# Kernel tuning notes

Measured on AMD Instinct MI355X. Metric: run time of the kernel, lower is better.

The kernel has to match this reference:

```python
import jax, jax.numpy as jnp
import numpy as np
from jax import lax

# pywt Wavelet('db4') decomposition filters
DEC_LO = jnp.array([-0.010597401784997278, 0.032883011666982945, 0.030841381835986965,
                    -0.18703481171888114, -0.02798376941698385, 0.6308807679295904,
                    0.7148465705525415, 0.23037781330885523], dtype=jnp.float32)
DEC_HI = jnp.array([-0.23037781330885523, 0.7148465705525415, -0.6308807679295904,
                    -0.02798376941698385, 0.18703481171888114, 0.030841381835986965,
                    -0.032883011666982945, -0.010597401784997278], dtype=jnp.float32)


def dwt_level(x, lo, hi):
    # single-level pywt dwt, mode='symmetric', along last axis
    f = lo.shape[0]
    p = f - 1
    pad = [(0, 0)] * (x.ndim - 1) + [(p, p)]
    xe = jnp.pad(x, pad, mode='symmetric')[..., 1:]  # offset 1 matches pywt phase
    lead = x.shape[:-1]
    xin = xe.reshape(-1, 1, xe.shape[-1])            # [N,1,L]
    filt = jnp.stack([lo[::-1], hi[::-1]])[:, None, :]  # flip: true convolution, [2,1,f]
    out = lax.conv_general_dilated(xin, filt, (2,), 'VALID')  # [N,2,floor((n+f-1)/2)]
    cA = out[:, 0].reshape(lead + (-1,))
    cD = out[:, 1].reshape(lead + (-1,))
    return cA, cD


def wavedec4(x):
    # pywt.wavedec(x,'db4',level=4) concatenated: [cA4,cD4,cD3,cD2,cD1]
    details = []
    a = x
    for _ in range(4):
        a, d = dwt_level(a, DEC_LO, DEC_HI)
        details.append(d)
    return jnp.concatenate([a] + details[::-1], axis=-1)


def lstm_last(xs, w_ih, w_hh, b_ih, b_hh):
    # torch LSTM (gate order i,f,g,o); returns last timestep hidden state
    B, T, _ = xs.shape
    H = w_hh.shape[1]
    h0 = jnp.zeros((B, H), xs.dtype)
    c0 = jnp.zeros((B, H), xs.dtype)
    b = b_ih + b_hh

    def step(carry, x_t):
        h, c = carry
        gates = x_t @ w_ih.T + h @ w_hh.T + b
        i, f, g, o = jnp.split(gates, 4, axis=-1)
        c = jax.nn.sigmoid(f) * c + jax.nn.sigmoid(i) * jnp.tanh(g)
        h = jax.nn.sigmoid(o) * jnp.tanh(c)
        return (h, c), None

    (h, _), _ = lax.scan(step, (h0, c0), jnp.swapaxes(xs, 0, 1))
    return h


def setup_inputs() -> dict:
    key = jax.random.key(0)
    ks = jax.random.split(key, 9)
    B, S, T = 256, 1024, 21
    return {
        'x': jax.random.normal(ks[0], (B, S, T), jnp.float32),
        'conv_w': jax.random.normal(ks[1], (64, 78, 3), jnp.float32) * 0.06,
        'conv_b': jax.random.normal(ks[2], (64,), jnp.float32) * 0.06,
        'w_ih': jax.random.normal(ks[3], (128, 64), jnp.float32) * 0.12,
        'w_hh': jax.random.normal(ks[4], (128, 32), jnp.float32) * 0.17,
        'b_ih': jax.random.normal(ks[5], (128,), jnp.float32) * 0.17,
        'b_hh': jax.random.normal(ks[6], (128,), jnp.float32) * 0.17,
        'fc_w': jax.random.normal(ks[7], (1, 32), jnp.float32) * 0.17,
        'fc_b': jax.random.normal(ks[8], (1,), jnp.float32) * 0.17,
    }


def reference(x, conv_w, conv_b, w_ih, w_hh, b_ih, b_hh, fc_w, fc_b):
    freq = jnp.abs(jnp.fft.rfft(x, axis=2))          # [B,S,11]
    tf = wavedec4(x)                                 # [B,S,46]
    combined = jnp.concatenate([x, freq, tf], axis=2)  # [B,S,78]
    combined = jnp.swapaxes(combined, 1, 2)          # [B,78,S]
    y = lax.conv_general_dilated(combined, conv_w, (1,), [(1, 1)]) + conv_b[None, :, None]
    y = jax.nn.relu(y)
    B, C, S = y.shape
    y = y.reshape(B, C, S // 2, 2).max(axis=-1)      # max_pool1d(k=2,s=2)
    y = jnp.transpose(y, (0, 2, 1))                  # [B,S//2,64]
    h = lstm_last(y, w_ih, w_hh, b_ih, b_hh)         # [B,32]
    return h @ fc_w.T + fc_b                         # [B,1]
```

## Files before the change

kernel.cpp:

```cpp
#include <hip/hip_runtime.h>
#include <math.h>

typedef _Float16 half8 __attribute__((ext_vector_type(8)));
typedef float floatx16 __attribute__((ext_vector_type(16)));
typedef float float2v __attribute__((ext_vector_type(2)));

constexpr float L2E = 1.4426950408889634f;

constexpr float DLO[8] = {-0.010597401784997278f, 0.032883011666982945f, 0.030841381835986965f,
                          -0.18703481171888114f, -0.02798376941698385f, 0.6308807679295904f,
                          0.7148465705525415f, 0.23037781330885523f};
constexpr float DHI[8] = {-0.23037781330885523f, 0.7148465705525415f, -0.6308807679295904f,
                          -0.02798376941698385f, 0.18703481171888114f, 0.030841381835986965f,
                          -0.032883011666982945f, -0.010597401784997278f};

constexpr float CT21[21] = {
  1.0f,          0.95557281f,  0.82623877f,  0.62348980f,  0.36534102f,  0.07473009f,
  -0.22252093f, -0.5f,        -0.73305187f, -0.90096887f, -0.98883083f,
  -0.98883083f, -0.90096887f, -0.73305187f, -0.5f,        -0.22252093f,
  0.07473009f,   0.36534102f,  0.62348980f,  0.82623877f,  0.95557281f};
constexpr float ST21[21] = {
  0.0f,          0.29475517f,  0.56332006f,  0.78183148f,  0.93087375f,  0.99720380f,
  0.97492791f,   0.86602540f,  0.68017274f,  0.43388374f,  0.14904227f,
  -0.14904227f, -0.43388374f, -0.68017274f, -0.86602540f, -0.97492791f,
  -0.99720380f, -0.93087375f, -0.78183148f, -0.56332006f, -0.29475517f};

template<int N>
__device__ __forceinline__ void dwt_step(const float* in, float* a, float* d) {
  constexpr int NO = (N + 7) / 2;
#pragma unroll
  for (int i = 0; i < NO; i++) {
    float sa = 0.f, sd = 0.f;
#pragma unroll
    for (int j = 0; j < 8; j++) {
      int rel = 2 * i + j - 6;
      int idx = (rel < 0) ? (-rel - 1) : ((rel >= N) ? (2 * N - rel - 1) : rel);
      float v = in[idx];
      sa = fmaf(v, DLO[7 - j], sa);
      sd = fmaf(v, DHI[7 - j], sd);
    }
    a[i] = sa;
    d[i] = sd;
  }
}

__device__ __forceinline__ void gload_lds16(const void* g, void* l) {
  __builtin_amdgcn_global_load_lds(
      (const __attribute__((address_space(1))) unsigned int*)g,
      (__attribute__((address_space(3))) unsigned int*)l, 16, 0, 0);
}

__device__ __forceinline__ void feature_row(const float* __restrict__ xr,
                                            _Float16* hrow) {
  float xx[21];
#pragma unroll
  for (int t = 0; t < 21; t++) xx[t] = xr[t];

#pragma unroll
  for (int i = 78; i < 88; i++) hrow[i] = (_Float16)0.f;

#pragma unroll
  for (int t = 0; t < 21; t++) hrow[t] = (_Float16)xx[t];

#pragma unroll
  for (int k = 0; k < 11; k++) {
    float re = 0.f, im = 0.f;
#pragma unroll
    for (int t = 0; t < 21; t++) {
      const int m = (k * t) % 21;
      re = fmaf(xx[t], CT21[m], re);
      im = fmaf(xx[t], ST21[m], im);
    }
    hrow[21 + k] = (_Float16)sqrtf(re * re + im * im);
  }

  float a1[14], d1[14];
  dwt_step<21>(xx, a1, d1);
#pragma unroll
  for (int i = 0; i < 14; i++) hrow[64 + i] = (_Float16)d1[i];
  float a2[10], d2[10];
  dwt_step<14>(a1, a2, d2);
#pragma unroll
  for (int i = 0; i < 10; i++) hrow[54 + i] = (_Float16)d2[i];
  float a3[8], d3[8];
  dwt_step<10>(a2, a3, d3);
#pragma unroll
  for (int i = 0; i < 8; i++) hrow[46 + i] = (_Float16)d3[i];
  float a4[7], d4[7];
  dwt_step<8>(a3, a4, d4);
#pragma unroll
  for (int i = 0; i < 7; i++) {
    hrow[32 + i] = (_Float16)a4[i];
    hrow[39 + i] = (_Float16)d4[i];
  }
}

__global__ __launch_bounds__(256) void wprep_kernel(const float* __restrict__ cw,
                                                    const float* __restrict__ w_ih,
                                                    const float* __restrict__ b_ih,
                                                    const float* __restrict__ b_hh,
                                                    _Float16* __restrict__ WbT,
                                                    _Float16* __restrict__ wih16,
                                                    float* __restrict__ biasI) {
  int idx = blockIdx.x * 256 + threadIdx.x;
  if (idx < 64 * 264) {
    int o = idx / 264, k = idx - o * 264;
    float v = 0.f;
    if (k < 240) {
      int dk = k / 80, c = k - dk * 80;
      if (c < 78) v = cw[o * 234 + c * 3 + dk];
    }
    WbT[idx] = (_Float16)v;
  } else if (idx < 16896 + 8192) {
    int j = idx - 16896;
    wih16[j] = (_Float16)(L2E * w_ih[j]);
  } else if (idx < 16896 + 8192 + 128) {
    int g = idx - 16896 - 8192;
    int p = ((g & 63) << 1) | (g >> 6);
    biasI[p] = L2E * (b_ih[g] + b_hh[g]);
  }
}

__global__ __launch_bounds__(256, 2) void conv_proj_kernel(const float* __restrict__ x,
                                                           const _Float16* __restrict__ WbT,
                                                           const float* __restrict__ cbias,
                                                           const _Float16* __restrict__ wih16,
                                                           const float* __restrict__ biasI,
                                                           float* __restrict__ Xp) {
  __shared__ __align__(16) char smem[61184];
  _Float16* At = (_Float16*)smem;
  _Float16* Bt = (_Float16*)(smem + 24576);
  _Float16* yt = (_Float16*)smem;
  _Float16* wl = (_Float16*)(smem + 9216);
  float* biasl = (float*)(smem + 27648);
  float* Xpt   = (float*)(smem + 28160);
  float* bl    = (float*)(smem + 60928);

  const int tid = threadIdx.x;
  const int b = blockIdx.y;
  const int s0 = blockIdx.x * 128;
  const int T0 = blockIdx.x * 64;

  {
    const char* srcB = (const char*)WbT;
#pragma unroll
    for (int i = 0; i < 8; i++) {
      const int idx = i * 256 + tid;
      gload_lds16(srcB + (size_t)idx * 16, (char*)Bt + (size_t)idx * 16);
    }
    if (tid < 64)
      gload_lds16(srcB + (size_t)(2048 + tid) * 16, (char*)Bt + (size_t)(2048 + tid) * 16);
  }
  if (tid < 64) bl[tid] = cbias[tid];

  if (tid < 130) {
    const int s = s0 - 1 + tid;
    __align__(16) _Float16 hrow[88];
    if (s < 0 || s > 1023) {
#pragma unroll
      for (int i = 0; i < 88; i++) hrow[i] = (_Float16)0.f;
    } else {
      feature_row(x + ((size_t)(b << 10) + s) * 21, hrow);
    }
    uint4* dst = (uint4*)&At[tid * 88];
    const uint4* src = (const uint4*)hrow;
#pragma unroll
    for (int i = 0; i < 11; i++) dst[i] = src[i];
  }
  __syncthreads();

  const int wave = tid >> 6, lane = tid & 63;
  const int ml = lane & 31;
  const int kg = lane >> 5;
  const int am = wave * 32 + ml;

  floatx16 acc0 = {};
  floatx16 acc1 = {};
#pragma unroll
  for (int ks = 0; ks < 15; ks++) {
    const int kb = ks * 16 + kg * 8;
    const int dk = (kb >= 160) ? 2 : ((kb >= 80) ? 1 : 0);
    const int c = kb - dk * 80;
    half8 av = *(const half8*)&At[(am + dk) * 88 + c];
    half8 bv0 = *(const half8*)&Bt[ml * 264 + kb];
    half8 bv1 = *(const half8*)&Bt[(32 + ml) * 264 + kb];
    acc0 = __builtin_amdgcn_mfma_f32_32x32x16_f16(av, bv0, acc0, 0, 0, 0);
    acc1 = __builtin_amdgcn_mfma_f32_32x32x16_f16(av, bv1, acc1, 0, 0, 0);
  }

  const float b0 = bl[ml], b1 = bl[32 + ml];
  float v0s[8], v1s[8];
#pragma unroll
  for (int p = 0; p < 8; p++) {
    v0s[p] = fmaxf(fmaxf(acc0[2 * p], acc0[2 * p + 1]) + b0, 0.f);
    v1s[p] = fmaxf(fmaxf(acc1[2 * p], acc1[2 * p + 1]) + b1, 0.f);
  }

  __syncthreads();

#pragma unroll
  for (int p = 0; p < 8; p++) {
    const int toff = (p & 1) + ((p >> 1) << 2);
    const int t = wave * 16 + (kg << 1) + toff;
    yt[t * 72 + ml] = (_Float16)v0s[p];
    yt[t * 72 + 32 + ml] = (_Float16)v1s[p];
  }
  for (int i = tid; i < 2048; i += 256) {
    int g = i >> 4, c4 = i & 15;
    *(uint2*)(wl + g * 72 + c4 * 4) = *(const uint2*)(wih16 + g * 64 + c4 * 4);
  }
  if (tid < 128) biasl[tid] = biasI[tid];
  __syncthreads();

  const int tm = wave & 1, tn0 = (wave >> 1) * 2;
  floatx16 pa0 = {};
  floatx16 pa1 = {};
#pragma unroll
  for (int kq = 0; kq < 4; kq++) {
    const int k0 = kq * 16 + kg * 8;
    half8 av = *(const half8*)&yt[(tm * 32 + ml) * 72 + k0];
    half8 bv0 = *(const half8*)&wl[(tn0 * 32 + ml) * 72 + k0];
    half8 bv1 = *(const half8*)&wl[((tn0 + 1) * 32 + ml) * 72 + k0];
    pa0 = __builtin_amdgcn_mfma_f32_32x32x16_f16(av, bv0, pa0, 0, 0, 0);
    pa1 = __builtin_amdgcn_mfma_f32_32x32x16_f16(av, bv1, pa1, 0, 0, 0);
  }

  {
    const int g0i = tn0 * 32 + ml;
    const int p0 = ((g0i & 63) << 1) | (g0i >> 6);
    const int g1i = (tn0 + 1) * 32 + ml;
    const int p1 = ((g1i & 63) << 1) | (g1i >> 6);
#pragma unroll
    for (int reg = 0; reg < 16; reg++) {
      const int row = (reg & 3) + 8 * (reg >> 2) + 4 * kg;
      const int m = tm * 32 + row;
      Xpt[m * 128 + p0] = pa0[reg];
      Xpt[m * 128 + p1] = pa1[reg];
    }
  }
  __syncthreads();

  float* xpg = Xp + ((size_t)b * 512 + T0) * 128;
  for (int i = tid; i < 2048; i += 256) {
    const int r = i >> 5, c4 = (i & 31) << 2;
    float4 v = *(float4*)&Xpt[r * 128 + c4];
    float4 bb = *(float4*)&biasl[c4];
    v.x += bb.x; v.y += bb.y; v.z += bb.z; v.w += bb.w;
    *(float4*)&xpg[r * 128 + c4] = v;
  }
}

__device__ __forceinline__ float bcast_lane(float v, int k) {
  return __uint_as_float(__builtin_amdgcn_readlane(__float_as_uint(v), k));
}

#if __has_builtin(__builtin_amdgcn_exp2f)
#define EXP2F __builtin_amdgcn_exp2f
#else
#define EXP2F exp2f
#endif

#if __has_builtin(__builtin_amdgcn_permlane32_swap)
__device__ __forceinline__ float swap_half(float x) {
  auto r = __builtin_amdgcn_permlane32_swap(__float_as_uint(x), __float_as_uint(x),
                                            false, false);
  return __uint_as_float(r[1]);
}
#else
__device__ __forceinline__ float swap_half(float x) { return __shfl_down(x, 32); }
#endif

__device__ __forceinline__ void lstm_step(float& h, float& c, float2v xg,
                                          const float* __restrict__ wA,
                                          const float* __restrict__ wB, bool lo) {
  float hs[32];
#pragma unroll
  for (int k = 0; k < 32; k++) hs[k] = bcast_lane(h, k);

  float aA0 = xg.x, aA1 = 0.f, aB0 = xg.y, aB1 = 0.f;
#pragma unroll
  for (int k = 0; k < 32; k += 2) {
    aA0 = fmaf(hs[k], wA[k], aA0);
    aB0 = fmaf(hs[k], wB[k], aB0);
    aA1 = fmaf(hs[k + 1], wA[k + 1], aA1);
    aB1 = fmaf(hs[k + 1], wB[k + 1], aB1);
  }
  const float gA = aA0 + aA1;
  const float gB = aB0 + aB1;

  float sA = __builtin_amdgcn_rcpf(1.0f + EXP2F(-gA));

  float argB = lo ? (gB + gB) : (-gB);
  float rB = __builtin_amdgcn_rcpf(EXP2F(argB) + 1.0f);
  float sB = lo ? fmaf(-2.f, rB, 1.f) : rB;

  float fv = swap_half(sA);
  float ov = swap_half(sB);
  c = fmaf(fv, c, sA * sB);
  float rc = __builtin_amdgcn_rcpf(EXP2F(c * (2.f * L2E)) + 1.0f);
  float ov2 = ov + ov;
  h = fmaf(-ov2, rc, ov);
}

__global__ __launch_bounds__(64, 1)
__attribute__((amdgpu_waves_per_eu(1, 1)))
void lstm_fc_kernel(const float* __restrict__ Xp,
                    const float* __restrict__ w_hh,
                    const float* __restrict__ fc_w,
                    const float* __restrict__ fc_b,
                    float* __restrict__ out) {
  const int b = blockIdx.x;
  const int L = threadIdx.x;
  const bool lo = (L < 32);

  float wA[32], wB[32];
  {
    const float4* rA = (const float4*)(w_hh + L * 32);
    const float4* rB = (const float4*)(w_hh + (L + 64) * 32);
#pragma unroll
    for (int q = 0; q < 8; q++) {
      float4 a4 = rA[q], b4 = rB[q];
      wA[4 * q + 0] = L2E * a4.x; wA[4 * q + 1] = L2E * a4.y;
      wA[4 * q + 2] = L2E * a4.z; wA[4 * q + 3] = L2E * a4.w;
      wB[4 * q + 0] = L2E * b4.x; wB[4 * q + 1] = L2E * b4.y;
      wB[4 * q + 2] = L2E * b4.z; wB[4 * q + 3] = L2E * b4.w;
    }
  }

  const float* xp = Xp + (size_t)b * 512 * 128;
  float h = 0.f, c = 0.f;

  float2v p2[4];
#pragma unroll
  for (int u = 0; u < 4; u++) p2[u] = *(const float2v*)&xp[u * 128 + 2 * L];

  for (int t0 = 0; t0 < 512; t0 += 4) {
    float2v c2[4];
#pragma unroll
    for (int u = 0; u < 4; u++) c2[u] = p2[u];
    if (t0 + 4 < 512) {
#pragma unroll
      for (int u = 0; u < 4; u++)
        p2[u] = *(const float2v*)&xp[(t0 + 4 + u) * 128 + 2 * L];
    }
#pragma unroll
    for (int u = 0; u < 4; u++) lstm_step(h, c, c2[u], wA, wB, lo);
  }

  float v = lo ? h * fc_w[L & 31] : 0.f;
#pragma unroll
  for (int off = 32; off > 0; off >>= 1) v += __shfl_down(v, off);
  if (L == 0) out[b] = v + fc_b[0];
}

extern "C" void kernel_launch(void* const* d_in, const int* in_sizes, int n_in,
                              void* d_out, int out_size, void* d_ws, size_t ws_size,
                              hipStream_t stream) {
  const float* x      = (const float*)d_in[0];
  const float* conv_w = (const float*)d_in[1];
  const float* conv_b = (const float*)d_in[2];
  const float* w_ih   = (const float*)d_in[3];
  const float* w_hh   = (const float*)d_in[4];
  const float* b_ih   = (const float*)d_in[5];
  const float* b_hh   = (const float*)d_in[6];
  const float* fc_w   = (const float*)d_in[7];
  const float* fc_b   = (const float*)d_in[8];
  float* out = (float*)d_out;

  char* wsb = (char*)d_ws;
  float*    Xp    = (float*)wsb;
  _Float16* WbT   = (_Float16*)(wsb + 67108864);
  _Float16* wih16 = (_Float16*)(wsb + 67108864 + 33792);
  float*    biasI = (float*)(wsb + 67108864 + 33792 + 16384);

  wprep_kernel<<<dim3(99), dim3(256), 0, stream>>>(conv_w, w_ih, b_ih, b_hh,
                                                   WbT, wih16, biasI);
  conv_proj_kernel<<<dim3(8, 256), dim3(256), 0, stream>>>(x, WbT, conv_b,
                                                           wih16, biasI, Xp);
  lstm_fc_kernel<<<dim3(256), dim3(64), 0, stream>>>(Xp, w_hh, fc_w, fc_b, out);
}
```

Baseline: 224.8 us.

## Fuse conv/projection and LSTM into one producer-consumer kernel per batch

Merges the conv+pool+input-projection kernel and the LSTM kernel into a single per-batch workgroup. Three producer waves compute 64-timestep chunks of projected gates while one consumer wave runs the LSTM recurrence on completed chunks, signalled through LDS atomic counters. The aim is to hide the conv/projection work behind the serial LSTM and drop a kernel launch. In exchange, the producer work for each batch now runs on three waves instead of eight blocks, and the sync relies on spin-waits and global-memory visibility within the workgroup.

Measured after the change: 199.4 us. -11.3%, faster.

```diff
diff --git a/kernel.cpp b/kernel.cpp
--- a/kernel.cpp
+++ b/kernel.cpp
@@ -121,13 +121,82 @@
   }
 }
 
-__global__ __launch_bounds__(256, 2) void conv_proj_kernel(const float* __restrict__ x,
-                                                           const _Float16* __restrict__ WbT,
-                                                           const float* __restrict__ cbias,
-                                                           const _Float16* __restrict__ wih16,
-                                                           const float* __restrict__ biasI,
-                                                           float* __restrict__ Xp) {
+__device__ __forceinline__ float bcast_lane(float v, int k) {
+  return __uint_as_float(__builtin_amdgcn_readlane(__float_as_uint(v), k));
+}
+
+#if __has_builtin(__builtin_amdgcn_exp2f)
+#define EXP2F __builtin_amdgcn_exp2f
+#else
+#define EXP2F exp2f
+#endif
+
+#if __has_builtin(__builtin_amdgcn_permlane32_swap)
+__device__ __forceinline__ float swap_half(float x) {
+  auto r = __builtin_amdgcn_permlane32_swap(__float_as_uint(x), __float_as_uint(x),
+                                            false, false);
+  return __uint_as_float(r[1]);
+}
+#else
+__device__ __forceinline__ float swap_half(float x) { return __shfl_down(x, 32); }
+#endif
+
+__device__ __forceinline__ void lstm_step(float& h, float& c, float2v xg,
+                                          const float* __restrict__ wA,
+                                          const float* __restrict__ wB, bool lo) {
+  float hs[32];
+#pragma unroll
+  for (int k = 0; k < 32; k++) hs[k] = bcast_lane(h, k);
+
+  float aA0 = xg.x, aA1 = 0.f, aB0 = xg.y, aB1 = 0.f;
+#pragma unroll
+  for (int k = 0; k < 32; k += 2) {
+    aA0 = fmaf(hs[k], wA[k], aA0);
+    aB0 = fmaf(hs[k], wB[k], aB0);
+    aA1 = fmaf(hs[k + 1], wA[k + 1], aA1);
+    aB1 = fmaf(hs[k + 1], wB[k + 1], aB1);
+  }
+  const float gA = aA0 + aA1;
+  const float gB = aB0 + aB1;
+
+  float sA = __builtin_amdgcn_rcpf(1.0f + EXP2F(-gA));
+
+  float argB = lo ? (gB + gB) : (-gB);
+  float rB = __builtin_amdgcn_rcpf(EXP2F(argB) + 1.0f);
+  float sB = lo ? fmaf(-2.f, rB, 1.f) : rB;
+
+  float fv = swap_half(sA);
+  float ov = swap_half(sB);
+  c = fmaf(fv, c, sA * sB);
+  float rc = __builtin_amdgcn_rcpf(EXP2F(c * (2.f * L2E)) + 1.0f);
+  float ov2 = ov + ov;
+  h = fmaf(-ov2, rc, ov);
+}
+
+__device__ __forceinline__ void prod_barrier(int* pb, int& target) {
+  target += 3;
+  __builtin_amdgcn_s_waitcnt(0);
+  if ((threadIdx.x & 63) == 0)
+    __hip_atomic_fetch_add(pb, 1, __ATOMIC_RELEASE, __HIP_MEMORY_SCOPE_WORKGROUP);
+  while (__hip_atomic_load(pb, __ATOMIC_ACQUIRE, __HIP_MEMORY_SCOPE_WORKGROUP) < target) {
+  }
+}
+
+__global__ __launch_bounds__(256, 1)
+__attribute__((amdgpu_waves_per_eu(1, 1)))
+void fused_kernel(const float* __restrict__ x,
+                  const _Float16* __restrict__ WbT,
+                  const float* __restrict__ cbias,
+                  const _Float16* __restrict__ wih16,
+                  const float* __restrict__ biasI,
+                  const float* __restrict__ w_hh,
+                  const float* __restrict__ fc_w,
+                  const float* __restrict__ fc_b,
+                  float* __restrict__ Xp,
+                  float* __restrict__ out) {
   __shared__ __align__(16) char smem[61184];
+  __shared__ int ready;
+  __shared__ int pbar;
   _Float16* At = (_Float16*)smem;
   _Float16* Bt = (_Float16*)(smem + 24576);
   _Float16* yt = (_Float16*)smem;
@@ -137,220 +206,166 @@
   float* bl    = (float*)(smem + 60928);
 
   const int tid = threadIdx.x;
-  const int b = blockIdx.y;
-  const int s0 = blockIdx.x * 128;
-  const int T0 = blockIdx.x * 64;
-
-  {
-    const char* srcB = (const char*)WbT;
-#pragma unroll
-    for (int i = 0; i < 8; i++) {
-      const int idx = i * 256 + tid;
-      gload_lds16(srcB + (size_t)idx * 16, (char*)Bt + (size_t)idx * 16);
-    }
-    if (tid < 64)
-      gload_lds16(srcB + (size_t)(2048 + tid) * 16, (char*)Bt + (size_t)(2048 + tid) * 16);
-  }
+  const int b = blockIdx.x;
+
+  if (tid == 0) { ready = 0; pbar = 0; }
   if (tid < 64) bl[tid] = cbias[tid];
-
-  if (tid < 130) {
-    const int s = s0 - 1 + tid;
-    __align__(16) _Float16 hrow[88];
-    if (s < 0 || s > 1023) {
-#pragma unroll
-      for (int i = 0; i < 88; i++) hrow[i] = (_Float16)0.f;
-    } else {
-      feature_row(x + ((size_t)(b << 10) + s) * 21, hrow);
-    }
-    uint4* dst = (uint4*)&At[tid * 88];
-    const uint4* src = (const uint4*)hrow;
-#pragma unroll
-    for (int i = 0; i < 11; i++) dst[i] = src[i];
-  }
   __syncthreads();
 
-  const int wave = tid >> 6, lane = tid & 63;
-  const int ml = lane & 31;
-  const int kg = lane >> 5;
-  const int am = wave * 32 + ml;
-
-  floatx16 acc0 = {};
-  floatx16 acc1 = {};
-#pragma unroll
-  for (int ks = 0; ks < 15; ks++) {
-    const int kb = ks * 16 + kg * 8;
-    const int dk = (kb >= 160) ? 2 : ((kb >= 80) ? 1 : 0);
-    const int c = kb - dk * 80;
-    half8 av = *(const half8*)&At[(am + dk) * 88 + c];
-    half8 bv0 = *(const half8*)&Bt[ml * 264 + kb];
-    half8 bv1 = *(const half8*)&Bt[(32 + ml) * 264 + kb];
-    acc0 = __builtin_amdgcn_mfma_f32_32x32x16_f16(av, bv0, acc0, 0, 0, 0);
-    acc1 = __builtin_amdgcn_mfma_f32_32x32x16_f16(av, bv1, acc1, 0, 0, 0);
-  }
-
-  const float b0 = bl[ml], b1 = bl[32 + ml];
-  float v0s[8], v1s[8];
-#pragma unroll
-  for (int p = 0; p < 8; p++) {
-    v0s[p] = fmaxf(fmaxf(acc0[2 * p], acc0[2 * p + 1]) + b0, 0.f);
-    v1s[p] = fmaxf(fmaxf(acc1[2 * p], acc1[2 * p + 1]) + b1, 0.f);
-  }
-
-  __syncthreads();
-
-#pragma unroll
-  for (int p = 0; p < 8; p++) {
-    const int toff = (p & 1) + ((p >> 1) << 2);
-    const int t = wave * 16 + (kg << 1) + toff;
-    yt[t * 72 + ml] = (_Float16)v0s[p];
-    yt[t * 72 + 32 + ml] = (_Float16)v1s[p];
-  }
-  for (int i = tid; i < 2048; i += 256) {
-    int g = i >> 4, c4 = i & 15;
-    *(uint2*)(wl + g * 72 + c4 * 4) = *(const uint2*)(wih16 + g * 64 + c4 * 4);
-  }
-  if (tid < 128) biasl[tid] = biasI[tid];
-  __syncthreads();
-
-  const int tm = wave & 1, tn0 = (wave >> 1) * 2;
-  floatx16 pa0 = {};
-  floatx16 pa1 = {};
-#pragma unroll
-  for (int kq = 0; kq < 4; kq++) {
-    const int k0 = kq * 16 + kg * 8;
-    half8 av = *(const half8*)&yt[(tm * 32 + ml) * 72 + k0];
-    half8 bv0 = *(const half8*)&wl[(tn0 * 32 + ml) * 72 + k0];
-    half8 bv1 = *(const half8*)&wl[((tn0 + 1) * 32 + ml) * 72 + k0];
-    pa0 = __builtin_amdgcn_mfma_f32_32x32x16_f16(av, bv0, pa0, 0, 0, 0);
-    pa1 = __builtin_amdgcn_mfma_f32_32x32x16_f16(av, bv1, pa1, 0, 0, 0);
-  }
-
-  {
-    const int g0i = tn0 * 32 + ml;
-    const int p0 = ((g0i & 63) << 1) | (g0i >> 6);
-    const int g1i = (tn0 + 1) * 32 + ml;
-    const int p1 = ((g1i & 63) << 1) | (g1i >> 6);
-#pragma unroll
-    for (int reg = 0; reg < 16; reg++) {
-      const int row = (reg & 3) + 8 * (reg >> 2) + 4 * kg;
-      const int m = tm * 32 + row;
-      Xpt[m * 128 + p0] = pa0[reg];
-      Xpt[m * 128 + p1] = pa1[reg];
-    }
-  }
-  __syncthreads();
-
-  float* xpg = Xp + ((size_t)b * 512 + T0) * 128;
-  for (int i = tid; i < 2048; i += 256) {
-    const int r = i >> 5, c4 = (i & 31) << 2;
-    float4 v = *(float4*)&Xpt[r * 128 + c4];
-    float4 bb = *(float4*)&biasl[c4];
-    v.x += bb.x; v.y += bb.y; v.z += bb.z; v.w += bb.w;
-    *(float4*)&xpg[r * 128 + c4] = v;
-  }
-}
-
-__device__ __forceinline__ float bcast_lane(float v, int k) {
-  return __uint_as_float(__builtin_amdgcn_readlane(__float_as_uint(v), k));
-}
-
-#if __has_builtin(__builtin_amdgcn_exp2f)
-#define EXP2F __builtin_amdgcn_exp2f
-#else
-#define EXP2F exp2f
-#endif
-
-#if __has_builtin(__builtin_amdgcn_permlane32_swap)
-__device__ __forceinline__ float swap_half(float x) {
-  auto r = __builtin_amdgcn_permlane32_swap(__float_as_uint(x), __float_as_uint(x),
-                                            false, false);
-  return __uint_as_float(r[1]);
-}
-#else
-__device__ __forceinline__ float swap_half(float x) { return __shfl_down(x, 32); }
-#endif
-
-__device__ __forceinline__ void lstm_step(float& h, float& c, float2v xg,
-                                          const float* __restrict__ wA,
-                                          const float* __restrict__ wB, bool lo) {
-  float hs[32];
-#pragma unroll
-  for (int k = 0; k < 32; k++) hs[k] = bcast_lane(h, k);
-
-  float aA0 = xg.x, aA1 = 0.f, aB0 = xg.y, aB1 = 0.f;
-#pragma unroll
-  for (int k = 0; k < 32; k += 2) {
-    aA0 = fmaf(hs[k], wA[k], aA0);
-    aB0 = fmaf(hs[k], wB[k], aB0);
-    aA1 = fmaf(hs[k + 1], wA[k + 1], aA1);
-    aB1 = fmaf(hs[k + 1], wB[k + 1], aB1);
-  }
-  const float gA = aA0 + aA1;
-  const float gB = aB0 + aB1;
-
-  float sA = __builtin_amdgcn_rcpf(1.0f + EXP2F(-gA));
-
-  float argB = lo ? (gB + gB) : (-gB);
-  float rB = __builtin_amdgcn_rcpf(EXP2F(argB) + 1.0f);
-  float sB = lo ? fmaf(-2.f, rB, 1.f) : rB;
-
-  float fv = swap_half(sA);
-  float ov = swap_half(sB);
-  c = fmaf(fv, c, sA * sB);
-  float rc = __builtin_amdgcn_rcpf(EXP2F(c * (2.f * L2E)) + 1.0f);
-  float ov2 = ov + ov;
-  h = fmaf(-ov2, rc, ov);
-}
-
-__global__ __launch_bounds__(64, 1)
-__attribute__((amdgpu_waves_per_eu(1, 1)))
-void lstm_fc_kernel(const float* __restrict__ Xp,
-                    const float* __restrict__ w_hh,
-                    const float* __restrict__ fc_w,
-                    const float* __restrict__ fc_b,
-                    float* __restrict__ out) {
-  const int b = blockIdx.x;
-  const int L = threadIdx.x;
-  const bool lo = (L < 32);
-
-  float wA[32], wB[32];
-  {
-    const float4* rA = (const float4*)(w_hh + L * 32);
-    const float4* rB = (const float4*)(w_hh + (L + 64) * 32);
-#pragma unroll
-    for (int q = 0; q < 8; q++) {
-      float4 a4 = rA[q], b4 = rB[q];
-      wA[4 * q + 0] = L2E * a4.x; wA[4 * q + 1] = L2E * a4.y;
-      wA[4 * q + 2] = L2E * a4.z; wA[4 * q + 3] = L2E * a4.w;
-      wB[4 * q + 0] = L2E * b4.x; wB[4 * q + 1] = L2E * b4.y;
-      wB[4 * q + 2] = L2E * b4.z; wB[4 * q + 3] = L2E * b4.w;
-    }
-  }
-
-  const float* xp = Xp + (size_t)b * 512 * 128;
-  float h = 0.f, c = 0.f;
-
-  float2v p2[4];
-#pragma unroll
-  for (int u = 0; u < 4; u++) p2[u] = *(const float2v*)&xp[u * 128 + 2 * L];
-
-  for (int t0 = 0; t0 < 512; t0 += 4) {
-    float2v c2[4];
-#pragma unroll
-    for (int u = 0; u < 4; u++) c2[u] = p2[u];
-    if (t0 + 4 < 512) {
-#pragma unroll
-      for (int u = 0; u < 4; u++)
-        p2[u] = *(const float2v*)&xp[(t0 + 4 + u) * 128 + 2 * L];
-    }
-#pragma unroll
-    for (int u = 0; u < 4; u++) lstm_step(h, c, c2[u], wA, wB, lo);
-  }
-
-  float v = lo ? h * fc_w[L & 31] : 0.f;
-#pragma unroll
-  for (int off = 32; off > 0; off >>= 1) v += __shfl_down(v, off);
-  if (L == 0) out[b] = v + fc_b[0];
+  if (tid < 64) {
+    const int L = tid;
+    const bool lo = (L < 32);
+    float wA[32], wB[32];
+    {
+      const float4* rA = (const float4*)(w_hh + L * 32);
+      const float4* rB = (const float4*)(w_hh + (L + 64) * 32);
+#pragma unroll
+      for (int q = 0; q < 8; q++) {
+        float4 a4 = rA[q], b4 = rB[q];
+        wA[4 * q + 0] = L2E * a4.x; wA[4 * q + 1] = L2E * a4.y;
+        wA[4 * q + 2] = L2E * a4.z; wA[4 * q + 3] = L2E * a4.w;
+        wB[4 * q + 0] = L2E * b4.x; wB[4 * q + 1] = L2E * b4.y;
+        wB[4 * q + 2] = L2E * b4.z; wB[4 * q + 3] = L2E * b4.w;
+      }
+    }
+
+    float h = 0.f, c = 0.f;
+    for (int k = 0; k < 8; k++) {
+      while (__hip_atomic_load(&ready, __ATOMIC_ACQUIRE, __HIP_MEMORY_SCOPE_WORKGROUP) < k + 1)
+        __builtin_amdgcn_s_sleep(2);
+      const float* xp = Xp + ((size_t)b * 512 + (size_t)k * 64) * 128;
+      float2v p2[4];
+#pragma unroll
+      for (int u = 0; u < 4; u++) p2[u] = *(const float2v*)&xp[u * 128 + 2 * L];
+      for (int t0 = 0; t0 < 64; t0 += 4) {
+        float2v c2[4];
+#pragma unroll
+        for (int u = 0; u < 4; u++) c2[u] = p2[u];
+        if (t0 + 4 < 64) {
+#pragma unroll
+          for (int u = 0; u < 4; u++)
+            p2[u] = *(const float2v*)&xp[(t0 + 4 + u) * 128 + 2 * L];
+        }
+#pragma unroll
+        for (int u = 0; u < 4; u++) lstm_step(h, c, c2[u], wA, wB, lo);
+      }
+    }
+
+    float v = lo ? h * fc_w[L & 31] : 0.f;
+#pragma unroll
+    for (int off = 32; off > 0; off >>= 1) v += __shfl_down(v, off);
+    if (L == 0) out[b] = v + fc_b[0];
+  } else {
+    const int ptid = tid - 64;
+    const int pw = (tid >> 6) - 1;
+    const int lane = tid & 63, ml = lane & 31, kg = lane >> 5;
+    int bt = 0;
+
+    for (int k = 0; k < 8; k++) {
+      const int s0 = k * 128;
+
+      {
+        const char* srcB = (const char*)WbT;
+#pragma unroll
+        for (int j = 0; j < 11; j++) {
+          const int idx = j * 192 + ptid;
+          gload_lds16(srcB + (size_t)idx * 16, (char*)Bt + (size_t)idx * 16);
+        }
+      }
+      if (ptid < 130) {
+        const int s = s0 - 1 + ptid;
+        __align__(16) _Float16 hrow[88];
+        if (s < 0 || s > 1023) {
+#pragma unroll
+          for (int i = 0; i < 88; i++) hrow[i] = (_Float16)0.f;
+        } else {
+          feature_row(x + ((size_t)(b << 10) + s) * 21, hrow);
+        }
+        uint4* dst = (uint4*)&At[ptid * 88];
+        const uint4* src = (const uint4*)hrow;
+#pragma unroll
+        for (int i = 0; i < 11; i++) dst[i] = src[i];
+      }
+      prod_barrier(&pbar, bt);
+
+      float pooled[3][8];
+      {
+        int cc = 0;
+        for (int wt = pw; wt < 8; wt += 3, cc++) {
+          const int mt = wt & 3, nt = wt >> 2;
+          floatx16 acc = {};
+#pragma unroll
+          for (int ks = 0; ks < 15; ks++) {
+            const int kb = ks * 16 + kg * 8;
+            const int dk = (kb >= 160) ? 2 : ((kb >= 80) ? 1 : 0);
+            const int cofs = kb - dk * 80;
+            half8 av = *(const half8*)&At[(mt * 32 + ml + dk) * 88 + cofs];
+            half8 bv = *(const half8*)&Bt[(nt * 32 + ml) * 264 + kb];
+            acc = __builtin_amdgcn_mfma_f32_32x32x16_f16(av, bv, acc, 0, 0, 0);
+          }
+          const float bo = bl[nt * 32 + ml];
+#pragma unroll
+          for (int p = 0; p < 8; p++)
+            pooled[cc][p] = fmaxf(fmaxf(acc[2 * p], acc[2 * p + 1]) + bo, 0.f);
+        }
+      }
+      prod_barrier(&pbar, bt);
+
+      {
+        int cc = 0;
+        for (int wt = pw; wt < 8; wt += 3, cc++) {
+          const int mt = wt & 3, nt = wt >> 2;
+#pragma unroll
+          for (int p = 0; p < 8; p++) {
+            const int toff = (p & 1) + ((p >> 1) << 2);
+            const int t = mt * 16 + (kg << 1) + toff;
+            yt[t * 72 + nt * 32 + ml] = (_Float16)pooled[cc][p];
+          }
+        }
+        for (int i = ptid; i < 2048; i += 192) {
+          int g = i >> 4, c4 = i & 15;
+          *(uint2*)(wl + g * 72 + c4 * 4) = *(const uint2*)(wih16 + g * 64 + c4 * 4);
+        }
+        if (ptid < 128) biasl[ptid] = biasI[ptid];
+      }
+      prod_barrier(&pbar, bt);
+
+      for (int wt = pw; wt < 8; wt += 3) {
+        const int pm = wt & 1, pn = wt >> 1;
+        floatx16 pa = {};
+#pragma unroll
+        for (int kq = 0; kq < 4; kq++) {
+          const int k0 = kq * 16 + kg * 8;
+          half8 av = *(const half8*)&yt[(pm * 32 + ml) * 72 + k0];
+          half8 bv = *(const half8*)&wl[(pn * 32 + ml) * 72 + k0];
+          pa = __builtin_amdgcn_mfma_f32_32x32x16_f16(av, bv, pa, 0, 0, 0);
+        }
+        const int gi = pn * 32 + ml;
+        const int pp = ((gi & 63) << 1) | (gi >> 6);
+#pragma unroll
+        for (int reg = 0; reg < 16; reg++) {
+          const int row = (reg & 3) + 8 * (reg >> 2) + 4 * kg;
+          Xpt[(pm * 32 + row) * 128 + pp] = pa[reg];
+        }
+      }
+      prod_barrier(&pbar, bt);
+
+      {
+        float* xpg = Xp + ((size_t)b * 512 + (size_t)k * 64) * 128;
+        for (int i = ptid; i < 2048; i += 192) {
+          const int r = i >> 5, c4 = (i & 31) << 2;
+          float4 v = *(float4*)&Xpt[r * 128 + c4];
+          float4 bb = *(float4*)&biasl[c4];
+          v.x += bb.x; v.y += bb.y; v.z += bb.z; v.w += bb.w;
+          *(float4*)&xpg[r * 128 + c4] = v;
+        }
+      }
+      prod_barrier(&pbar, bt);
+
+      if (tid == 64)
+        __hip_atomic_fetch_add(&ready, 1, __ATOMIC_RELEASE, __HIP_MEMORY_SCOPE_WORKGROUP);
+    }
+  }
 }
 
 extern "C" void kernel_launch(void* const* d_in, const int* in_sizes, int n_in,
@@ -375,7 +390,6 @@
 
   wprep_kernel<<<dim3(99), dim3(256), 0, stream>>>(conv_w, w_ih, b_ih, b_hh,
                                                    WbT, wih16, biasI);
-  conv_proj_kernel<<<dim3(8, 256), dim3(256), 0, stream>>>(x, WbT, conv_b,
-                                                           wih16, biasI, Xp);
-  lstm_fc_kernel<<<dim3(256), dim3(64), 0, stream>>>(Xp, w_hh, fc_w, fc_b, out);
-}
+  fused_kernel<<<dim3(256), dim3(256), 0, stream>>>(x, WbT, conv_b, wih16, biasI,
+                                                    w_hh, fc_w, fc_b, Xp, out);
+}
```
